# Optimization experiments

Measured on AMD Instinct MI355X. Metric: run time of the kernel, lower is better.

The kernel has to match this reference:

```python
import jax, jax.numpy as jnp
import numpy as np

N_GROUPS = 4
N_CODES = 160
EMBED_DIM = 512
GROUP_DIM = EMBED_DIM // N_GROUPS  # 128


def setup_inputs() -> dict:
    key = jax.random.key(0)
    k1, k2 = jax.random.split(key)
    B, T = 16, 4096
    xin = jax.random.normal(k1, (B, EMBED_DIM, T), dtype=jnp.float32)
    # matches nn.Embedding init: uniform(-1/n_e, 1/n_e)
    codebook = jax.random.uniform(k2, (N_GROUPS, N_CODES, GROUP_DIM), dtype=jnp.float32,
                                  minval=-1.0 / N_CODES, maxval=1.0 / N_CODES)
    return {"xin": xin, "codebook": codebook}


def _quantize(xin, codebook):
    B, C, T = xin.shape
    x_btc = jnp.transpose(xin, (0, 2, 1))            # [B, T, C]
    x = x_btc.reshape(-1, N_GROUPS, GROUP_DIM)       # [N, G, D]
    # squared euclidean distance per group: [N, G, K]
    d = (jnp.sum(x ** 2, axis=-1, keepdims=True)
         + jnp.sum(codebook ** 2, axis=-1)[None, :, :]
         - 2.0 * jnp.einsum('ngd,gkd->ngk', x, codebook))
    idx = jnp.argmin(d, axis=-1)                     # [N, G] int
    # gather codewords: [N, G, D]
    z_q = jnp.take_along_axis(codebook[None], idx[:, :, None, None], axis=2)[:, :, 0, :]
    z_q = z_q.reshape(B, T, C)                       # [B, T, C]
    return x_btc, z_q, idx.reshape(B, T, N_GROUPS)


def reference(xin, codebook):
    B, C, T = xin.shape
    x_btc, z_q, codes = _quantize(xin, codebook)
    sg = jax.lax.stop_gradient
    loss = 0.25 * jnp.mean((sg(z_q) - x_btc) ** 2) + jnp.mean((z_q - sg(x_btc)) ** 2)
    z_q_st = x_btc + sg(z_q - x_btc)                 # straight-through
    z_q_out = jnp.transpose(z_q_st, (0, 2, 1))       # [B, C, T]
    codes_out = jnp.transpose(codes, (0, 2, 1))      # [B, G, T]
    return z_q_out, loss, codes_out
```

## Files before the change

kernel.cpp:

```cpp
#include <hip/hip_runtime.h>
#include <stdint.h>

#define NG 4
#define NK 160
#define GD 128
#define ED 512
#define BB 16
#define TT 4096
#define BK 32
#define BTOK 256
static constexpr size_t ZSZ = (size_t)BB * ED * TT;

typedef float f32x4 __attribute__((ext_vector_type(4)));


__global__ void prep_kernel(const float* __restrict__ cb, float* __restrict__ sc,
                            float* __restrict__ ct) {
  int i = blockIdx.x * 256 + threadIdx.x;
  int g = i / (GD * NK), r = i % (GD * NK), d = r / NK, k = r % NK;
  ct[i] = cb[((size_t)g * NK + k) * GD + d];
  if (i < NG * NK) {
    const float* c = cb + (size_t)i * GD;
    float s = 0.f;
    for (int dd = 0; dd < GD; ++dd) s = fmaf(c[dd], c[dd], s);
    sc[i] = s;
  }
}

__global__ __launch_bounds__(512) void vq_kernel(const float* __restrict__ xin,
                                                 const float* __restrict__ cb,
                                                 const float* __restrict__ sc,
                                                 const float* __restrict__ ct,
                                                 float* __restrict__ out,
                                                 float* __restrict__ bsum) {
  __shared__ __align__(16) float xs[BK * BTOK];
  __shared__ float wred[4];

  const int tid = (int)threadIdx.x;
  const int w = tid >> 6;
  const int l = tid & 63;
  const int g = (int)(blockIdx.x >> 8);
  const int tb = (int)(blockIdx.x & 255);
  const int b = tb >> 4;
  const int t0 = (tb & 15) << 8;

  const float* xbase = xin + ((size_t)(b * ED + g * GD)) * TT + t0;
  const float* ctg = ct + (size_t)g * GD * NK;
  const int kbase = __builtin_amdgcn_readfirstlane(w) * 20;

  float acc[4][20];
#pragma unroll
  for (int i = 0; i < 4; ++i)
#pragma unroll
    for (int j = 0; j < 20; ++j) acc[i][j] = 0.f;
  float sxa[4] = {0.f, 0.f, 0.f, 0.f};

  for (int k0 = 0; k0 < GD; k0 += BK) {
    __syncthreads();
#pragma unroll
    for (int i = 0; i < 4; ++i) {
      int q = i * 512 + tid;
      int dd = q >> 6, col = (q & 63) << 2;
      *(f32x4*)&xs[dd * BTOK + col] =
          *(const f32x4*)(xbase + (size_t)(k0 + dd) * TT + col);
    }
    __syncthreads();

#pragma unroll 2
    for (int dd = 0; dd < BK; ++dd) {
      const f32x4 xv = *(const f32x4*)&xs[dd * BTOK + l * 4];
      const float* cw = ctg + (size_t)(k0 + dd) * NK + kbase;
      const f32x4 c0 = *(const f32x4*)&cw[0];
      const f32x4 c1 = *(const f32x4*)&cw[4];
      const f32x4 c2 = *(const f32x4*)&cw[8];
      const f32x4 c3 = *(const f32x4*)&cw[12];
      const f32x4 c4 = *(const f32x4*)&cw[16];
#pragma unroll
      for (int i = 0; i < 4; ++i) sxa[i] = fmaf(xv[i], xv[i], sxa[i]);
#pragma unroll
      for (int i = 0; i < 4; ++i) {
        const float xf = xv[i];
#pragma unroll
        for (int e = 0; e < 4; ++e) {
          acc[i][e] = fmaf(xf, c0[e], acc[i][e]);
          acc[i][4 + e] = fmaf(xf, c1[e], acc[i][4 + e]);
          acc[i][8 + e] = fmaf(xf, c2[e], acc[i][8 + e]);
          acc[i][12 + e] = fmaf(xf, c3[e], acc[i][12 + e]);
          acc[i][16 + e] = fmaf(xf, c4[e], acc[i][16 + e]);
        }
      }
    }
  }

  const float* scw = sc + g * NK + kbase;
  float best[4] = {3.4e38f, 3.4e38f, 3.4e38f, 3.4e38f};
  int bik[4] = {0, 0, 0, 0};
#pragma unroll
  for (int j = 0; j < 20; ++j) {
    const float scv = scw[j];
#pragma unroll
    for (int i = 0; i < 4; ++i) {
      const float dv = (sxa[i] + scv) - 2.0f * acc[i][j];
      if (dv < best[i]) { best[i] = dv; bik[i] = kbase + j; }
    }
  }

  __syncthreads();
  float* bestW = xs;
  int* bikW = (int*)(xs + 2048);
  *(f32x4*)&bestW[w * 256 + l * 4] = (f32x4){best[0], best[1], best[2], best[3]};
#pragma unroll
  for (int i = 0; i < 4; ++i) bikW[w * 256 + l * 4 + i] = bik[i];
  __syncthreads();

  if (tid < 256) {
    float bf = bestW[tid];
    int kf = bikW[tid];
#pragma unroll
    for (int ww = 1; ww < 8; ++ww) {
      float bw = bestW[ww * 256 + tid];
      int kw = bikW[ww * 256 + tid];
      if (bw < bf) { bf = bw; kf = kw; }
    }

    out[ZSZ + 1 + ((size_t)(b * NG + g)) * TT + t0 + tid] = (float)kf;

    const f32x4* cw = (const f32x4*)(cb + ((size_t)g * NK + kf) * GD);
    float* zbase = out + ((size_t)(b * ED + g * GD)) * TT + t0 + tid;
#pragma unroll 4
    for (int d4 = 0; d4 < 32; ++d4) {
      f32x4 v = cw[d4];
      zbase[(size_t)(4 * d4 + 0) * TT] = v[0];
      zbase[(size_t)(4 * d4 + 1) * TT] = v[1];
      zbase[(size_t)(4 * d4 + 2) * TT] = v[2];
      zbase[(size_t)(4 * d4 + 3) * TT] = v[3];
    }

    float s = bf;
#pragma unroll
    for (int off = 32; off > 0; off >>= 1) s += __shfl_down(s, off, 64);
    if (l == 0) wred[w] = s;
  }
  __syncthreads();
  if (tid == 0)
    bsum[blockIdx.x] = ((wred[0] + wred[1]) + wred[2]) + wred[3];
}

__global__ __launch_bounds__(64) void loss_kernel(const float* __restrict__ bsum,
                                                  float* __restrict__ out) {
  float s = 0.f;
  for (int j = 0; j < 16; ++j) s += bsum[threadIdx.x + 64 * j];
#pragma unroll
  for (int off = 32; off > 0; off >>= 1) s += __shfl_down(s, off, 64);
  if (threadIdx.x == 0) out[ZSZ] = 1.25f * s / (float)ZSZ;
}

extern "C" void kernel_launch(void* const* d_in, const int* in_sizes, int n_in,
                              void* d_out, int out_size, void* d_ws, size_t ws_size,
                              hipStream_t stream) {
  const float* xin = (const float*)d_in[0];
  const float* cb  = (const float*)d_in[1];
  float* out  = (float*)d_out;
  float* bsum = (float*)d_ws;
  float* sc   = (float*)d_ws + 1024;
  float* ct   = (float*)d_ws + 2048;

  prep_kernel<<<320, 256, 0, stream>>>(cb, sc, ct);
  vq_kernel<<<1024, 512, 0, stream>>>(xin, cb, sc, ct, out, bsum);
  loss_kernel<<<1, 64, 0, stream>>>(bsum, out);
}
```

Baseline: 143.9 us.

## Double-buffer x tiles in LDS and split codeword writeback across all threads

Adds a second LDS buffer and prefetches the next 32-row x slab into registers while the current slab is being used for the distance FMAs. This overlaps global loads with compute and removes one barrier per k-step. The codeword gather and z_q writeback is now split across all 512 threads, each handling half the dimensions, instead of only 256 threads. The cost is doubled LDS use, which may lower occupancy, and extra registers for the prefetch staging.

```diff
diff --git a/kernel.cpp b/kernel.cpp
--- a/kernel.cpp
+++ b/kernel.cpp
@@ -33,7 +33,8 @@
                                                  const float* __restrict__ ct,
                                                  float* __restrict__ out,
                                                  float* __restrict__ bsum) {
-  __shared__ __align__(16) float xs[BK * BTOK];
+  __shared__ __align__(16) float xs[2][BK * BTOK];
+  __shared__ int kfS[BTOK];
   __shared__ float wred[4];
 
   const int tid = (int)threadIdx.x;
@@ -48,6 +49,19 @@
   const float* ctg = ct + (size_t)g * GD * NK;
   const int kbase = __builtin_amdgcn_readfirstlane(w) * 20;
 
+  f32x4 st[4];
+#pragma unroll
+  for (int i = 0; i < 4; ++i) {
+    int q = i * 512 + tid, dd = q >> 6, col = (q & 63) << 2;
+    st[i] = *(const f32x4*)(xbase + (size_t)dd * TT + col);
+  }
+#pragma unroll
+  for (int i = 0; i < 4; ++i) {
+    int q = i * 512 + tid, dd = q >> 6, col = (q & 63) << 2;
+    *(f32x4*)&xs[0][dd * BTOK + col] = st[i];
+  }
+  __syncthreads();
+
   float acc[4][20];
 #pragma unroll
   for (int i = 0; i < 4; ++i)
@@ -55,21 +69,19 @@
     for (int j = 0; j < 20; ++j) acc[i][j] = 0.f;
   float sxa[4] = {0.f, 0.f, 0.f, 0.f};
 
-  for (int k0 = 0; k0 < GD; k0 += BK) {
-    __syncthreads();
+  for (int s = 0; s < 4; ++s) {
+    const int cur = s & 1;
+    if (s < 3) {
 #pragma unroll
-    for (int i = 0; i < 4; ++i) {
-      int q = i * 512 + tid;
-      int dd = q >> 6, col = (q & 63) << 2;
-      *(f32x4*)&xs[dd * BTOK + col] =
-          *(const f32x4*)(xbase + (size_t)(k0 + dd) * TT + col);
+      for (int i = 0; i < 4; ++i) {
+        int q = i * 512 + tid, dd = q >> 6, col = (q & 63) << 2;
+        st[i] = *(const f32x4*)(xbase + (size_t)((s + 1) * BK + dd) * TT + col);
+      }
     }
-    __syncthreads();
-
 #pragma unroll 2
     for (int dd = 0; dd < BK; ++dd) {
-      const f32x4 xv = *(const f32x4*)&xs[dd * BTOK + l * 4];
-      const float* cw = ctg + (size_t)(k0 + dd) * NK + kbase;
+      const f32x4 xv = *(const f32x4*)&xs[cur][dd * BTOK + l * 4];
+      const float* cw = ctg + (size_t)(s * BK + dd) * NK + kbase;
       const f32x4 c0 = *(const f32x4*)&cw[0];
       const f32x4 c1 = *(const f32x4*)&cw[4];
       const f32x4 c2 = *(const f32x4*)&cw[8];
@@ -90,6 +102,14 @@
         }
       }
     }
+    if (s < 3) {
+#pragma unroll
+      for (int i = 0; i < 4; ++i) {
+        int q = i * 512 + tid, dd = q >> 6, col = (q & 63) << 2;
+        *(f32x4*)&xs[cur ^ 1][dd * BTOK + col] = st[i];
+      }
+      __syncthreads();
+    }
   }
 
   const float* scw = sc + g * NK + kbase;
@@ -106,8 +126,8 @@
   }
 
   __syncthreads();
-  float* bestW = xs;
-  int* bikW = (int*)(xs + 2048);
+  float* bestW = xs[0];
+  int* bikW = (int*)xs[0] + 2048;
   *(f32x4*)&bestW[w * 256 + l * 4] = (f32x4){best[0], best[1], best[2], best[3]};
 #pragma unroll
   for (int i = 0; i < 4; ++i) bikW[w * 256 + l * 4 + i] = bik[i];
@@ -122,19 +142,9 @@
       int kw = bikW[ww * 256 + tid];
       if (bw < bf) { bf = bw; kf = kw; }
     }
+    kfS[tid] = kf;
 
     out[ZSZ + 1 + ((size_t)(b * NG + g)) * TT + t0 + tid] = (float)kf;
-
-    const f32x4* cw = (const f32x4*)(cb + ((size_t)g * NK + kf) * GD);
-    float* zbase = out + ((size_t)(b * ED + g * GD)) * TT + t0 + tid;
-#pragma unroll 4
-    for (int d4 = 0; d4 < 32; ++d4) {
-      f32x4 v = cw[d4];
-      zbase[(size_t)(4 * d4 + 0) * TT] = v[0];
-      zbase[(size_t)(4 * d4 + 1) * TT] = v[1];
-      zbase[(size_t)(4 * d4 + 2) * TT] = v[2];
-      zbase[(size_t)(4 * d4 + 3) * TT] = v[3];
-    }
 
     float s = bf;
 #pragma unroll
@@ -142,6 +152,24 @@
     if (l == 0) wred[w] = s;
   }
   __syncthreads();
+
+  {
+    const int tok = tid & 255;
+    const int half = tid >> 8;
+    const int kf = kfS[tok];
+    const f32x4* cw = (const f32x4*)(cb + ((size_t)g * NK + kf) * GD) + half * 16;
+    float* zbase = out + ((size_t)(b * ED + g * GD) + (size_t)half * 64) * TT
+                   + t0 + tok;
+#pragma unroll 4
+    for (int d4 = 0; d4 < 16; ++d4) {
+      f32x4 v = cw[d4];
+      zbase[(size_t)(4 * d4 + 0) * TT] = v[0];
+      zbase[(size_t)(4 * d4 + 1) * TT] = v[1];
+      zbase[(size_t)(4 * d4 + 2) * TT] = v[2];
+      zbase[(size_t)(4 * d4 + 3) * TT] = v[3];
+    }
+  }
+
   if (tid == 0)
     bsum[blockIdx.x] = ((wred[0] + wred[1]) + wred[2]) + wred[3];
 }
```

After: 146.3 us. Within noise of the previous version (+1.6%).

## Halve tokens per block and spread codeword writeback across all threads

Applied to the files above, without the earlier changes.

Each block now handles 128 tokens instead of 256, and each thread accumulates 2 tokens instead of 4. This doubles the grid to 2048 blocks and cuts accumulator register pressure. The z_q writeback is now spread over all 512 threads, each writing a quarter of the dimensions, instead of 256 threads writing all 128. The cost is that every codebook column load from global memory is amortized over half as many tokens, and the loss reduction has twice as many partial sums.

```diff
diff --git a/kernel.cpp b/kernel.cpp
--- a/kernel.cpp
+++ b/kernel.cpp
@@ -8,10 +8,11 @@
 #define BB 16
 #define TT 4096
 #define BK 32
-#define BTOK 256
+#define WTOK 128
 static constexpr size_t ZSZ = (size_t)BB * ED * TT;
 
 typedef float f32x4 __attribute__((ext_vector_type(4)));
+typedef float f32x2 __attribute__((ext_vector_type(2)));
 
 
 __global__ void prep_kernel(const float* __restrict__ cb, float* __restrict__ sc,
@@ -33,52 +34,53 @@
                                                  const float* __restrict__ ct,
                                                  float* __restrict__ out,
                                                  float* __restrict__ bsum) {
-  __shared__ __align__(16) float xs[BK * BTOK];
-  __shared__ float wred[4];
+  __shared__ __align__(16) float xs[BK * WTOK];
+  __shared__ int kfS[WTOK];
+  __shared__ float wred[2];
 
   const int tid = (int)threadIdx.x;
   const int w = tid >> 6;
   const int l = tid & 63;
-  const int g = (int)(blockIdx.x >> 8);
-  const int tb = (int)(blockIdx.x & 255);
-  const int b = tb >> 4;
-  const int t0 = (tb & 15) << 8;
+  const int g = (int)(blockIdx.x >> 9);
+  const int tb = (int)(blockIdx.x & 511);
+  const int b = tb >> 5;
+  const int t0 = (tb & 31) << 7;
 
   const float* xbase = xin + ((size_t)(b * ED + g * GD)) * TT + t0;
   const float* ctg = ct + (size_t)g * GD * NK;
   const int kbase = __builtin_amdgcn_readfirstlane(w) * 20;
 
-  float acc[4][20];
+  float acc[2][20];
 #pragma unroll
-  for (int i = 0; i < 4; ++i)
+  for (int i = 0; i < 2; ++i)
 #pragma unroll
     for (int j = 0; j < 20; ++j) acc[i][j] = 0.f;
-  float sxa[4] = {0.f, 0.f, 0.f, 0.f};
+  float sxa[2] = {0.f, 0.f};
 
-  for (int k0 = 0; k0 < GD; k0 += BK) {
+  for (int s = 0; s < 4; ++s) {
     __syncthreads();
 #pragma unroll
-    for (int i = 0; i < 4; ++i) {
+    for (int i = 0; i < 2; ++i) {
       int q = i * 512 + tid;
-      int dd = q >> 6, col = (q & 63) << 2;
-      *(f32x4*)&xs[dd * BTOK + col] =
-          *(const f32x4*)(xbase + (size_t)(k0 + dd) * TT + col);
+      int dd = q >> 5, col = (q & 31) << 2;
+      *(f32x4*)&xs[dd * WTOK + col] =
+          *(const f32x4*)(xbase + (size_t)(s * BK + dd) * TT + col);
     }
     __syncthreads();
 
-#pragma unroll 2
+#pragma unroll 4
     for (int dd = 0; dd < BK; ++dd) {
-      const f32x4 xv = *(const f32x4*)&xs[dd * BTOK + l * 4];
-      const float* cw = ctg + (size_t)(k0 + dd) * NK + kbase;
+      const f32x2 xv = *(const f32x2*)&xs[dd * WTOK + l * 2];
+      const float* cw = ctg + (size_t)(s * BK + dd) * NK + kbase;
       const f32x4 c0 = *(const f32x4*)&cw[0];
       const f32x4 c1 = *(const f32x4*)&cw[4];
       const f32x4 c2 = *(const f32x4*)&cw[8];
       const f32x4 c3 = *(const f32x4*)&cw[12];
       const f32x4 c4 = *(const f32x4*)&cw[16];
 #pragma unroll
-      for (int i = 0; i < 4; ++i) sxa[i] = fmaf(xv[i], xv[i], sxa[i]);
+      for (int i = 0; i < 2; ++i) sxa[i] = fmaf(xv[i], xv[i], sxa[i]);
 #pragma unroll
-      for (int i = 0; i < 4; ++i) {
+      for (int i = 0; i < 2; ++i) {
         const float xf = xv[i];
 #pragma unroll
         for (int e = 0; e < 4; ++e) {
@@ -93,13 +95,13 @@
   }
 
   const float* scw = sc + g * NK + kbase;
-  float best[4] = {3.4e38f, 3.4e38f, 3.4e38f, 3.4e38f};
-  int bik[4] = {0, 0, 0, 0};
+  float best[2] = {3.4e38f, 3.4e38f};
+  int bik[2] = {0, 0};
 #pragma unroll
   for (int j = 0; j < 20; ++j) {
     const float scv = scw[j];
 #pragma unroll
-    for (int i = 0; i < 4; ++i) {
+    for (int i = 0; i < 2; ++i) {
       const float dv = (sxa[i] + scv) - 2.0f * acc[i][j];
       if (dv < best[i]) { best[i] = dv; bik[i] = kbase + j; }
     }
@@ -107,34 +109,24 @@
 
   __syncthreads();
   float* bestW = xs;
-  int* bikW = (int*)(xs + 2048);
-  *(f32x4*)&bestW[w * 256 + l * 4] = (f32x4){best[0], best[1], best[2], best[3]};
-#pragma unroll
-  for (int i = 0; i < 4; ++i) bikW[w * 256 + l * 4 + i] = bik[i];
+  int* bikW = (int*)xs + 1024;
+  *(f32x2*)&bestW[w * WTOK + l * 2] = (f32x2){best[0], best[1]};
+  bikW[w * WTOK + l * 2] = bik[0];
+  bikW[w * WTOK + l * 2 + 1] = bik[1];
   __syncthreads();
 
-  if (tid < 256) {
+  if (tid < WTOK) {
     float bf = bestW[tid];
     int kf = bikW[tid];
 #pragma unroll
     for (int ww = 1; ww < 8; ++ww) {
-      float bw = bestW[ww * 256 + tid];
-      int kw = bikW[ww * 256 + tid];
+      float bw = bestW[ww * WTOK + tid];
+      int kw = bikW[ww * WTOK + tid];
       if (bw < bf) { bf = bw; kf = kw; }
     }
+    kfS[tid] = kf;
 
     out[ZSZ + 1 + ((size_t)(b * NG + g)) * TT + t0 + tid] = (float)kf;
-
-    const f32x4* cw = (const f32x4*)(cb + ((size_t)g * NK + kf) * GD);
-    float* zbase = out + ((size_t)(b * ED + g * GD)) * TT + t0 + tid;
-#pragma unroll 4
-    for (int d4 = 0; d4 < 32; ++d4) {
-      f32x4 v = cw[d4];
-      zbase[(size_t)(4 * d4 + 0) * TT] = v[0];
-      zbase[(size_t)(4 * d4 + 1) * TT] = v[1];
-      zbase[(size_t)(4 * d4 + 2) * TT] = v[2];
-      zbase[(size_t)(4 * d4 + 3) * TT] = v[3];
-    }
 
     float s = bf;
 #pragma unroll
@@ -142,14 +134,31 @@
     if (l == 0) wred[w] = s;
   }
   __syncthreads();
-  if (tid == 0)
-    bsum[blockIdx.x] = ((wred[0] + wred[1]) + wred[2]) + wred[3];
+
+  {
+    const int tok = tid & 127;
+    const int quarter = tid >> 7;
+    const int kf = kfS[tok];
+    const f32x4* cw = (const f32x4*)(cb + ((size_t)g * NK + kf) * GD) + quarter * 8;
+    float* zbase = out + ((size_t)(b * ED + g * GD) + (size_t)quarter * 32) * TT
+                   + t0 + tok;
+#pragma unroll 4
+    for (int d4 = 0; d4 < 8; ++d4) {
+      f32x4 v = cw[d4];
+      zbase[(size_t)(4 * d4 + 0) * TT] = v[0];
+      zbase[(size_t)(4 * d4 + 1) * TT] = v[1];
+      zbase[(size_t)(4 * d4 + 2) * TT] = v[2];
+      zbase[(size_t)(4 * d4 + 3) * TT] = v[3];
+    }
+  }
+
+  if (tid == 0) bsum[blockIdx.x] = wred[0] + wred[1];
 }
 
 __global__ __launch_bounds__(64) void loss_kernel(const float* __restrict__ bsum,
                                                   float* __restrict__ out) {
   float s = 0.f;
-  for (int j = 0; j < 16; ++j) s += bsum[threadIdx.x + 64 * j];
+  for (int j = 0; j < 32; ++j) s += bsum[threadIdx.x + 64 * j];
 #pragma unroll
   for (int off = 32; off > 0; off >>= 1) s += __shfl_down(s, off, 64);
   if (threadIdx.x == 0) out[ZSZ] = 1.25f * s / (float)ZSZ;
@@ -162,10 +171,10 @@
   const float* cb  = (const float*)d_in[1];
   float* out  = (float*)d_out;
   float* bsum = (float*)d_ws;
-  float* sc   = (float*)d_ws + 1024;
-  float* ct   = (float*)d_ws + 2048;
+  float* sc   = (float*)d_ws + 2048;
+  float* ct   = (float*)d_ws + 4096;
 
   prep_kernel<<<320, 256, 0, stream>>>(cb, sc, ct);
-  vq_kernel<<<1024, 512, 0, stream>>>(xin, cb, sc, ct, out, bsum);
+  vq_kernel<<<2048, 512, 0, stream>>>(xin, cb, sc, ct, out, bsum);
   loss_kernel<<<1, 64, 0, stream>>>(bsum, out);
 }
```

Result: faster. 132.4 us (-8.0%).
